# Optimization experiments

Measured on AMD Instinct MI355X. Metric: run time of the kernel, lower is better.

The kernel has to match this reference:

```python
import jax, jax.numpy as jnp
import numpy as np

TAU = 2.0          # LIF membrane time constant
V_TH = 1.0         # spike threshold (spikingjelly default)
BN_EPS = 1e-5

T, C_IN, C_OUT, L = 16, 512, 512, 4096


def setup_inputs() -> dict:
    key = jax.random.key(0)
    k1, k2 = jax.random.split(key)
    x = jax.random.normal(k1, (T, C_IN, L), dtype=jnp.float32)
    W = jax.random.normal(k2, (C_OUT, C_IN), dtype=jnp.float32) * 0.02
    gamma = jnp.ones((C_OUT,), dtype=jnp.float32)
    beta = jnp.zeros((C_OUT,), dtype=jnp.float32)
    return {"x": x, "W": W, "gamma": gamma, "beta": beta}


def reference(x, W, gamma, beta):
    # 1x1 Conv1d (bias=False): [T, Cin, L] x [Cout, Cin] -> [T, Cout, L]
    y = jnp.einsum("tcl,oc->tol", x, W)

    # BatchNorm1d in training mode: normalize per channel over (T, L)
    mean = jnp.mean(y, axis=(0, 2), keepdims=True)
    var = jnp.mean(jnp.square(y - mean), axis=(0, 2), keepdims=True)  # biased var
    y = (y - mean) * jax.lax.rsqrt(var + BN_EPS)
    y = y * gamma[None, :, None] + beta[None, :, None]

    # Multi-step LIF: v' = v + (x - v)/tau ; spike = H(v' - vth) ; hard reset to 0
    def step(v, x_t):
        v = v + (x_t - v) / TAU
        s = (v >= V_TH).astype(v.dtype)
        v = v * (1.0 - s)  # v_reset = 0
        return v, s

    v0 = jnp.zeros_like(y[0])
    _, spikes = jax.lax.scan(step, v0, y)
    return spikes
```

## Files before the change

### kernel.cpp

```cpp
#include <hip/hip_runtime.h>


#define T_STEPS 16
#define CIN 512
#define COUT 512
#define LDIM 4096
#define KB 16
#define NL (COUT * LDIM)

static constexpr size_t NY = (size_t)T_STEPS * NL;

__device__ float g_yf[NY];
__device__ float g_mr[2 * COUT];
__device__ int   g_bf16;

__device__ __forceinline__ float b2f(unsigned short u) {
    return __uint_as_float(((unsigned int)u) << 16);
}

__global__ void detect_dtype(const unsigned int* __restrict__ gamma_words) {
    if (threadIdx.x == 0)
        g_bf16 = (gamma_words[0] == 0x3F803F80u) ? 1 : 0;
}

__global__ __launch_bounds__(256) void gemm_np(
    const void* __restrict__ xin, const void* __restrict__ win,
    float* __restrict__ yws, int use_ws)
{
#pragma clang fp contract(off)
    float* __restrict__ y = use_ws ? yws : g_yf;
    const int bf = g_bf16;

    __shared__ float Ws[KB][64];
    __shared__ float Xs[KB][64];

    const int lb = blockIdx.x * 64;
    const int ob = blockIdx.y * 64;
    const int t  = blockIdx.z;

    const int tid = threadIdx.x;
    const int tx = tid & 15;
    const int ty = tid >> 4;

    float acc[4][4];
    #pragma unroll
    for (int i = 0; i < 4; i++)
        #pragma unroll
        for (int j = 0; j < 4; j++) acc[i][j] = 0.0f;

    const int wrow = tid >> 2;
    const int wcol = (tid & 3) * 4;
    const int xrow = tid >> 4;
    const int xcol = (tid & 15) * 4;

    const size_t woff = (size_t)(ob + wrow) * CIN;
    const size_t xoff = (size_t)t * CIN * LDIM;

    for (int k0 = 0; k0 < CIN; k0 += KB) {
        float w0, w1, w2, w3, x0, x1, x2, x3;
        if (bf) {
            ushort4 wf = *reinterpret_cast<const ushort4*>(
                (const unsigned short*)win + woff + k0 + wcol);
            ushort4 xf = *reinterpret_cast<const ushort4*>(
                (const unsigned short*)xin + xoff + (size_t)(k0 + xrow) * LDIM + lb + xcol);
            w0 = b2f(wf.x); w1 = b2f(wf.y); w2 = b2f(wf.z); w3 = b2f(wf.w);
            x0 = b2f(xf.x); x1 = b2f(xf.y); x2 = b2f(xf.z); x3 = b2f(xf.w);
        } else {
            float4 wf = *reinterpret_cast<const float4*>(
                (const float*)win + woff + k0 + wcol);
            float4 xf = *reinterpret_cast<const float4*>(
                (const float*)xin + xoff + (size_t)(k0 + xrow) * LDIM + lb + xcol);
            w0 = wf.x; w1 = wf.y; w2 = wf.z; w3 = wf.w;
            x0 = xf.x; x1 = xf.y; x2 = xf.z; x3 = xf.w;
        }
        __syncthreads();
        Ws[wcol + 0][wrow] = w0; Ws[wcol + 1][wrow] = w1;
        Ws[wcol + 2][wrow] = w2; Ws[wcol + 3][wrow] = w3;
        Xs[xrow][xcol + 0] = x0; Xs[xrow][xcol + 1] = x1;
        Xs[xrow][xcol + 2] = x2; Xs[xrow][xcol + 3] = x3;
        __syncthreads();
        #pragma unroll
        for (int kk = 0; kk < KB; ++kk) {
            const float4 wv = *reinterpret_cast<const float4*>(&Ws[kk][ty * 4]);
            const float4 xv = *reinterpret_cast<const float4*>(&Xs[kk][tx * 4]);
            const float wr[4] = {wv.x, wv.y, wv.z, wv.w};
            const float xr[4] = {xv.x, xv.y, xv.z, xv.w};
            #pragma unroll
            for (int i = 0; i < 4; i++)
                #pragma unroll
                for (int j = 0; j < 4; j++)
                    acc[i][j] = acc[i][j] + wr[i] * xr[j];
        }
    }

    #pragma unroll
    for (int i = 0; i < 4; i++) {
        size_t row = (size_t)t * COUT + ob + ty * 4 + i;
        float* yp = &y[row * LDIM + lb + tx * 4];
        #pragma unroll
        for (int j = 0; j < 4; j++) yp[j] = acc[i][j];
    }
}

__global__ __launch_bounds__(256) void bn_stats_np(
    const float* __restrict__ yws, int use_ws)
{
#pragma clang fp contract(off)
    const float* __restrict__ y = use_ws ? yws : g_yf;
    const int o = blockIdx.x;
    const int g = threadIdx.x >> 3;
    const int l = threadIdx.x & 7;

    __shared__ float leaves[32];
    __shared__ float mean_sh;
    __shared__ float acc_sh[2];

    for (int phase = 0; phase < 2; ++phase) {
        __syncthreads();
        const float mean = (phase == 1) ? mean_sh : 0.0f;
        for (int t = 0; t < T_STEPS; ++t) {
            const float* row = &y[(size_t)t * NL + (size_t)o * LDIM + g * 128];
            float r[8];
            #pragma unroll
            for (int q = 0; q < 8; q++) {
                float a = row[q * 8 + l];
                float b = row[64 + q * 8 + l];
                if (phase == 1) {
                    float da = a - mean; a = da * da;
                    float db = b - mean; b = db * db;
                }
                r[q] = a + b;
            }
            float s01 = r[0] + r[1], s23 = r[2] + r[3];
            float s45 = r[4] + r[5], s67 = r[6] + r[7];
            float S = (s01 + s23) + (s45 + s67);
            S = S + __shfl_xor(S, 1);
            S = S + __shfl_xor(S, 2);
            S = S + __shfl_xor(S, 4);
            __syncthreads();
            if (l == 0) leaves[g] = S;
            __syncthreads();
            if (threadIdx.x == 0) {
                float a16[16], a8[8], a4[4], a2[2];
                #pragma unroll
                for (int k = 0; k < 16; k++) a16[k] = leaves[2*k] + leaves[2*k+1];
                #pragma unroll
                for (int k = 0; k < 8;  k++) a8[k] = a16[2*k] + a16[2*k+1];
                #pragma unroll
                for (int k = 0; k < 4;  k++) a4[k] = a8[2*k] + a8[2*k+1];
                #pragma unroll
                for (int k = 0; k < 2;  k++) a2[k] = a4[2*k] + a4[2*k+1];
                float pw = a2[0] + a2[1];
                if (t == 0) acc_sh[phase] = pw;
                else        acc_sh[phase] = acc_sh[phase] + pw;
            }
            __syncthreads();
        }
        if (threadIdx.x == 0) {
            if (phase == 0) {
                mean_sh = __fdiv_rn(acc_sh[0], 65536.0f);
            } else {
                float var = __fdiv_rn(acc_sh[1], 65536.0f);
                float rr = __fdiv_rn(1.0f, __fsqrt_rn(var + 1e-5f));
                g_mr[o] = mean_sh;
                g_mr[COUT + o] = rr;
            }
        }
    }
}

__global__ __launch_bounds__(256) void lif_np(
    const void* __restrict__ gin, const void* __restrict__ bin,
    void* __restrict__ outv, const float* __restrict__ yws, int use_ws)
{
#pragma clang fp contract(off)
    const float* __restrict__ y = use_ws ? yws : g_yf;
    const int bf = g_bf16;
    const int idx = blockIdx.x * 256 + threadIdx.x;
    const int o = idx >> 12;
    const float mean = g_mr[o];
    const float r    = g_mr[COUT + o];
    float gm, bt;
    if (bf) {
        gm = b2f(((const unsigned short*)gin)[o]);
        bt = b2f(((const unsigned short*)bin)[o]);
    } else {
        gm = ((const float*)gin)[o];
        bt = ((const float*)bin)[o];
    }
    float v = 0.0f;
    #pragma unroll
    for (int t = 0; t < T_STEPS; t++) {
        float yv = y[(size_t)t * NL + idx];
        float d  = yv - mean;
        float n1 = d * r;
        float n2 = n1 * gm;
        float n3 = n2 + bt;
        float dv = n3 - v;
        float h  = dv * 0.5f;
        v = v + h;
        float s;
        if (v >= 1.0f) { s = 1.0f; v = 0.0f; } else { s = 0.0f; }
        if (bf) ((unsigned short*)outv)[(size_t)t * NL + idx] = (s == 1.0f) ? 0x3F80 : 0x0000;
        else    ((float*)outv)[(size_t)t * NL + idx] = s;
    }
}

extern "C" void kernel_launch(void* const* d_in, const int* in_sizes, int n_in,
                              void* d_out, int out_size, void* d_ws, size_t ws_size,
                              hipStream_t stream) {
    const void* x     = d_in[0];
    const void* W     = d_in[1];
    const void* gamma = d_in[2];
    const void* beta  = d_in[3];

    const int use_ws = (ws_size >= NY * sizeof(float)) ? 1 : 0;
    float* yws = (float*)d_ws;

    detect_dtype<<<1, 64, 0, stream>>>((const unsigned int*)gamma);

    dim3 grid(LDIM / 64, COUT / 64, T_STEPS);
    gemm_np<<<grid, 256, 0, stream>>>(x, W, yws, use_ws);

    bn_stats_np<<<COUT, 256, 0, stream>>>(yws, use_ws);

    lif_np<<<NL / 256, 256, 0, stream>>>(gamma, beta, d_out, yws, use_ws);
}
```

Measured before the change: 915.4 us.

## Widen GEMM tile to 64x128 with packed float2 math and K-block 32

Each thread of the conv GEMM now computes a 4x8 output tile instead of 4x4, the K block doubles to 32, and global loads and stores are wider. The inner product uses two-wide float vectors, which the compiler can map to AMD packed FP32 instructions, so fewer issue slots are spent per FMA. The goal is less shared-memory traffic per flop and higher arithmetic throughput in the dominant GEMM. In exchange it uses more registers and shared memory, which may lower occupancy, and it halves the number of blocks.

```diff
diff --git a/kernel.cpp b/kernel.cpp
--- a/kernel.cpp
+++ b/kernel.cpp
@@ -5,8 +5,10 @@
 #define CIN 512
 #define COUT 512
 #define LDIM 4096
-#define KB 16
+#define KB 32
 #define NL (COUT * LDIM)
+
+typedef float v2f __attribute__((ext_vector_type(2)));
 
 static constexpr size_t NY = (size_t)T_STEPS * NL;
 
@@ -16,6 +18,12 @@
 
 __device__ __forceinline__ float b2f(unsigned short u) {
     return __uint_as_float(((unsigned int)u) << 16);
+}
+__device__ __forceinline__ float blo(unsigned int u) {
+    return __uint_as_float(u << 16);
+}
+__device__ __forceinline__ float bhi(unsigned int u) {
+    return __uint_as_float(u & 0xFFFF0000u);
 }
 
 __global__ void detect_dtype(const unsigned int* __restrict__ gamma_words) {
@@ -32,9 +40,9 @@
     const int bf = g_bf16;
 
     __shared__ float Ws[KB][64];
-    __shared__ float Xs[KB][64];
-
-    const int lb = blockIdx.x * 64;
+    __shared__ float Xs[KB][128];
+
+    const int lb = blockIdx.x * 128;
     const int ob = blockIdx.y * 64;
     const int t  = blockIdx.z;
 
@@ -42,63 +50,86 @@
     const int tx = tid & 15;
     const int ty = tid >> 4;
 
-    float acc[4][4];
+    const int wrow = tid >> 2;
+    const int wk   = (tid & 3) * 8;
+    const int xk   = tid >> 3;
+    const int xl   = (tid & 7) * 16;
+
+    const size_t wbase = (size_t)(ob + wrow) * CIN + wk;
+    const size_t xbase = (size_t)t * CIN * LDIM + (size_t)xk * LDIM + lb + xl;
+
+    v2f acc[4][4];
     #pragma unroll
     for (int i = 0; i < 4; i++)
         #pragma unroll
-        for (int j = 0; j < 4; j++) acc[i][j] = 0.0f;
-
-    const int wrow = tid >> 2;
-    const int wcol = (tid & 3) * 4;
-    const int xrow = tid >> 4;
-    const int xcol = (tid & 15) * 4;
-
-    const size_t woff = (size_t)(ob + wrow) * CIN;
-    const size_t xoff = (size_t)t * CIN * LDIM;
+        for (int j = 0; j < 4; j++) acc[i][j] = (v2f)(0.0f);
 
     for (int k0 = 0; k0 < CIN; k0 += KB) {
-        float w0, w1, w2, w3, x0, x1, x2, x3;
+        float wv[8], xv[16];
         if (bf) {
-            ushort4 wf = *reinterpret_cast<const ushort4*>(
-                (const unsigned short*)win + woff + k0 + wcol);
-            ushort4 xf = *reinterpret_cast<const ushort4*>(
-                (const unsigned short*)xin + xoff + (size_t)(k0 + xrow) * LDIM + lb + xcol);
-            w0 = b2f(wf.x); w1 = b2f(wf.y); w2 = b2f(wf.z); w3 = b2f(wf.w);
-            x0 = b2f(xf.x); x1 = b2f(xf.y); x2 = b2f(xf.z); x3 = b2f(xf.w);
+            uint4 wu = *reinterpret_cast<const uint4*>(
+                (const unsigned short*)win + wbase + k0);
+            uint4 xu0 = *reinterpret_cast<const uint4*>(
+                (const unsigned short*)xin + xbase + (size_t)k0 * LDIM);
+            uint4 xu1 = *reinterpret_cast<const uint4*>(
+                (const unsigned short*)xin + xbase + (size_t)k0 * LDIM + 8);
+            wv[0]=blo(wu.x); wv[1]=bhi(wu.x); wv[2]=blo(wu.y); wv[3]=bhi(wu.y);
+            wv[4]=blo(wu.z); wv[5]=bhi(wu.z); wv[6]=blo(wu.w); wv[7]=bhi(wu.w);
+            xv[0]=blo(xu0.x); xv[1]=bhi(xu0.x); xv[2]=blo(xu0.y); xv[3]=bhi(xu0.y);
+            xv[4]=blo(xu0.z); xv[5]=bhi(xu0.z); xv[6]=blo(xu0.w); xv[7]=bhi(xu0.w);
+            xv[8]=blo(xu1.x); xv[9]=bhi(xu1.x); xv[10]=blo(xu1.y); xv[11]=bhi(xu1.y);
+            xv[12]=blo(xu1.z); xv[13]=bhi(xu1.z); xv[14]=blo(xu1.w); xv[15]=bhi(xu1.w);
         } else {
-            float4 wf = *reinterpret_cast<const float4*>(
-                (const float*)win + woff + k0 + wcol);
-            float4 xf = *reinterpret_cast<const float4*>(
-                (const float*)xin + xoff + (size_t)(k0 + xrow) * LDIM + lb + xcol);
-            w0 = wf.x; w1 = wf.y; w2 = wf.z; w3 = wf.w;
-            x0 = xf.x; x1 = xf.y; x2 = xf.z; x3 = xf.w;
+            float4 w0 = *reinterpret_cast<const float4*>((const float*)win + wbase + k0);
+            float4 w1 = *reinterpret_cast<const float4*>((const float*)win + wbase + k0 + 4);
+            wv[0]=w0.x; wv[1]=w0.y; wv[2]=w0.z; wv[3]=w0.w;
+            wv[4]=w1.x; wv[5]=w1.y; wv[6]=w1.z; wv[7]=w1.w;
+            #pragma unroll
+            for (int m = 0; m < 4; m++) {
+                float4 xf = *reinterpret_cast<const float4*>(
+                    (const float*)xin + xbase + (size_t)k0 * LDIM + m * 4);
+                xv[m*4+0]=xf.x; xv[m*4+1]=xf.y; xv[m*4+2]=xf.z; xv[m*4+3]=xf.w;
+            }
         }
         __syncthreads();
-        Ws[wcol + 0][wrow] = w0; Ws[wcol + 1][wrow] = w1;
-        Ws[wcol + 2][wrow] = w2; Ws[wcol + 3][wrow] = w3;
-        Xs[xrow][xcol + 0] = x0; Xs[xrow][xcol + 1] = x1;
-        Xs[xrow][xcol + 2] = x2; Xs[xrow][xcol + 3] = x3;
+        #pragma unroll
+        for (int m = 0; m < 8; m++) Ws[wk + m][wrow] = wv[m];
+        #pragma unroll
+        for (int m = 0; m < 4; m++) {
+            float4 st = {xv[m*4+0], xv[m*4+1], xv[m*4+2], xv[m*4+3]};
+            *reinterpret_cast<float4*>(&Xs[xk][xl + m * 4]) = st;
+        }
         __syncthreads();
+
         #pragma unroll
         for (int kk = 0; kk < KB; ++kk) {
-            const float4 wv = *reinterpret_cast<const float4*>(&Ws[kk][ty * 4]);
-            const float4 xv = *reinterpret_cast<const float4*>(&Xs[kk][tx * 4]);
-            const float wr[4] = {wv.x, wv.y, wv.z, wv.w};
-            const float xr[4] = {xv.x, xv.y, xv.z, xv.w};
+            const float4 w4 = *reinterpret_cast<const float4*>(&Ws[kk][ty * 4]);
+            const float4 xa = *reinterpret_cast<const float4*>(&Xs[kk][tx * 8]);
+            const float4 xb = *reinterpret_cast<const float4*>(&Xs[kk][tx * 8 + 4]);
+            v2f xp[4];
+            xp[0] = (v2f){xa.x, xa.y}; xp[1] = (v2f){xa.z, xa.w};
+            xp[2] = (v2f){xb.x, xb.y}; xp[3] = (v2f){xb.z, xb.w};
+            const float wr[4] = {w4.x, w4.y, w4.z, w4.w};
             #pragma unroll
-            for (int i = 0; i < 4; i++)
-                #pragma unroll
-                for (int j = 0; j < 4; j++)
-                    acc[i][j] = acc[i][j] + wr[i] * xr[j];
+            for (int i = 0; i < 4; i++) {
+                v2f wp = (v2f){wr[i], wr[i]};
+                #pragma unroll
+                for (int j = 0; j < 4; j++) {
+                    v2f p = wp * xp[j];
+                    acc[i][j] = acc[i][j] + p;
+                }
+            }
         }
     }
 
     #pragma unroll
     for (int i = 0; i < 4; i++) {
         size_t row = (size_t)t * COUT + ob + ty * 4 + i;
-        float* yp = &y[row * LDIM + lb + tx * 4];
-        #pragma unroll
-        for (int j = 0; j < 4; j++) yp[j] = acc[i][j];
+        float* yp = &y[row * LDIM + lb + tx * 8];
+        float4 s0 = {acc[i][0].x, acc[i][0].y, acc[i][1].x, acc[i][1].y};
+        float4 s1 = {acc[i][2].x, acc[i][2].y, acc[i][3].x, acc[i][3].y};
+        *reinterpret_cast<float4*>(yp) = s0;
+        *reinterpret_cast<float4*>(yp + 4) = s1;
     }
 }
 
@@ -219,7 +250,7 @@
 
     detect_dtype<<<1, 64, 0, stream>>>((const unsigned int*)gamma);
 
-    dim3 grid(LDIM / 64, COUT / 64, T_STEPS);
+    dim3 grid(LDIM / 128, COUT / 64, T_STEPS);
     gemm_np<<<grid, 256, 0, stream>>>(x, W, yws, use_ws);
 
     bn_stats_np<<<COUT, 256, 0, stream>>>(yws, use_ws);
```

New measurement: 885.2 us. -3.3%, faster.

## Replace shared-memory tiled GEMM with per-thread column GEMM using transposed weights

Applied to the files above, without the earlier changes.

Adds a kernel that transposes W into a global k-major buffer, then replaces the LDS-tiled 64x64 GEMM with a kernel where each thread owns one L position and accumulates 32 output channels. The weight reads are the same for every thread in a block, so they become uniform (scalar or broadcast) loads, and x is streamed coalesced straight from global memory. This removes the shared-memory staging and barriers. The cost is that each x element is reloaded for every 32-channel group, which multiplies global and L2 traffic for x, and each block reuses much less data than before.

```diff
diff --git a/kernel.cpp b/kernel.cpp
--- a/kernel.cpp
+++ b/kernel.cpp
@@ -5,12 +5,12 @@
 #define CIN 512
 #define COUT 512
 #define LDIM 4096
-#define KB 16
 #define NL (COUT * LDIM)
 
 static constexpr size_t NY = (size_t)T_STEPS * NL;
 
 __device__ float g_yf[NY];
+__device__ float g_wt[CIN * COUT];
 __device__ float g_mr[2 * COUT];
 __device__ int   g_bf16;
 
@@ -23,83 +23,60 @@
         g_bf16 = (gamma_words[0] == 0x3F803F80u) ? 1 : 0;
 }
 
-__global__ __launch_bounds__(256) void gemm_np(
-    const void* __restrict__ xin, const void* __restrict__ win,
-    float* __restrict__ yws, int use_ws)
+__global__ __launch_bounds__(256) void wrepack(const void* __restrict__ win) {
+    const int idx = blockIdx.x * 256 + threadIdx.x;
+    const int k = idx >> 9;
+    const int o = idx & 511;
+    float v;
+    if (g_bf16) v = b2f(((const unsigned short*)win)[(size_t)o * CIN + k]);
+    else        v = ((const float*)win)[(size_t)o * CIN + k];
+    g_wt[(size_t)k * COUT + o] = v;
+}
+
+__global__ __launch_bounds__(256) void gemm_sg(
+    const void* __restrict__ xin, float* __restrict__ yws, int use_ws)
 {
 #pragma clang fp contract(off)
     float* __restrict__ y = use_ws ? yws : g_yf;
     const int bf = g_bf16;
 
-    __shared__ float Ws[KB][64];
-    __shared__ float Xs[KB][64];
-
-    const int lb = blockIdx.x * 64;
-    const int ob = blockIdx.y * 64;
+    const int l  = blockIdx.x * 256 + threadIdx.x;
+    const int og = blockIdx.y;
     const int t  = blockIdx.z;
 
-    const int tid = threadIdx.x;
-    const int tx = tid & 15;
-    const int ty = tid >> 4;
-
-    float acc[4][4];
+    float acc[32];
     #pragma unroll
-    for (int i = 0; i < 4; i++)
-        #pragma unroll
-        for (int j = 0; j < 4; j++) acc[i][j] = 0.0f;
-
-    const int wrow = tid >> 2;
-    const int wcol = (tid & 3) * 4;
-    const int xrow = tid >> 4;
-    const int xcol = (tid & 15) * 4;
-
-    const size_t woff = (size_t)(ob + wrow) * CIN;
-    const size_t xoff = (size_t)t * CIN * LDIM;
-
-    for (int k0 = 0; k0 < CIN; k0 += KB) {
-        float w0, w1, w2, w3, x0, x1, x2, x3;
-        if (bf) {
-            ushort4 wf = *reinterpret_cast<const ushort4*>(
-                (const unsigned short*)win + woff + k0 + wcol);
-            ushort4 xf = *reinterpret_cast<const ushort4*>(
-                (const unsigned short*)xin + xoff + (size_t)(k0 + xrow) * LDIM + lb + xcol);
-            w0 = b2f(wf.x); w1 = b2f(wf.y); w2 = b2f(wf.z); w3 = b2f(wf.w);
-            x0 = b2f(xf.x); x1 = b2f(xf.y); x2 = b2f(xf.z); x3 = b2f(xf.w);
-        } else {
-            float4 wf = *reinterpret_cast<const float4*>(
-                (const float*)win + woff + k0 + wcol);
-            float4 xf = *reinterpret_cast<const float4*>(
-                (const float*)xin + xoff + (size_t)(k0 + xrow) * LDIM + lb + xcol);
-            w0 = wf.x; w1 = wf.y; w2 = wf.z; w3 = wf.w;
-            x0 = xf.x; x1 = xf.y; x2 = xf.z; x3 = xf.w;
-        }
-        __syncthreads();
-        Ws[wcol + 0][wrow] = w0; Ws[wcol + 1][wrow] = w1;
-        Ws[wcol + 2][wrow] = w2; Ws[wcol + 3][wrow] = w3;
-        Xs[xrow][xcol + 0] = x0; Xs[xrow][xcol + 1] = x1;
-        Xs[xrow][xcol + 2] = x2; Xs[xrow][xcol + 3] = x3;
-        __syncthreads();
-        #pragma unroll
-        for (int kk = 0; kk < KB; ++kk) {
-            const float4 wv = *reinterpret_cast<const float4*>(&Ws[kk][ty * 4]);
-            const float4 xv = *reinterpret_cast<const float4*>(&Xs[kk][tx * 4]);
-            const float wr[4] = {wv.x, wv.y, wv.z, wv.w};
-            const float xr[4] = {xv.x, xv.y, xv.z, xv.w};
+    for (int i = 0; i < 32; i++) acc[i] = 0.0f;
+
+    const float* __restrict__ wt = g_wt + og * 32;
+
+    if (bf) {
+        const unsigned short* __restrict__ xp =
+            (const unsigned short*)xin + (size_t)t * CIN * LDIM + l;
+        #pragma unroll 2
+        for (int k = 0; k < CIN; k++) {
+            const float xv = b2f(xp[(size_t)k * LDIM]);
+            const float* __restrict__ wr = wt + (size_t)k * COUT;
             #pragma unroll
-            for (int i = 0; i < 4; i++)
-                #pragma unroll
-                for (int j = 0; j < 4; j++)
-                    acc[i][j] = acc[i][j] + wr[i] * xr[j];
-        }
-    }
-
+            for (int i = 0; i < 32; i++)
+                acc[i] = acc[i] + wr[i] * xv;
+        }
+    } else {
+        const float* __restrict__ xp =
+            (const float*)xin + (size_t)t * CIN * LDIM + l;
+        #pragma unroll 2
+        for (int k = 0; k < CIN; k++) {
+            const float xv = xp[(size_t)k * LDIM];
+            const float* __restrict__ wr = wt + (size_t)k * COUT;
+            #pragma unroll
+            for (int i = 0; i < 32; i++)
+                acc[i] = acc[i] + wr[i] * xv;
+        }
+    }
+
+    float* __restrict__ yp = y + ((size_t)t * COUT + og * 32) * LDIM + l;
     #pragma unroll
-    for (int i = 0; i < 4; i++) {
-        size_t row = (size_t)t * COUT + ob + ty * 4 + i;
-        float* yp = &y[row * LDIM + lb + tx * 4];
-        #pragma unroll
-        for (int j = 0; j < 4; j++) yp[j] = acc[i][j];
-    }
+    for (int i = 0; i < 32; i++) yp[(size_t)i * LDIM] = acc[i];
 }
 
 __global__ __launch_bounds__(256) void bn_stats_np(
@@ -219,8 +196,10 @@
 
     detect_dtype<<<1, 64, 0, stream>>>((const unsigned int*)gamma);
 
-    dim3 grid(LDIM / 64, COUT / 64, T_STEPS);
-    gemm_np<<<grid, 256, 0, stream>>>(x, W, yws, use_ws);
+    wrepack<<<(CIN * COUT) / 256, 256, 0, stream>>>(W);
+
+    dim3 grid(LDIM / 256, COUT / 32, T_STEPS);
+    gemm_sg<<<grid, 256, 0, stream>>>(x, yws, use_ws);
 
     bn_stats_np<<<COUT, 256, 0, stream>>>(yws, use_ws);
 
```

Measured after the change: 816.1 us. 1.12x faster.
